# Performance work log

Measured on AMD Instinct MI355X. Metric: run time of the kernel, lower is better.

## Reference

```python
import jax, jax.numpy as jnp
import numpy as np

EPS = 1e-7   # GENConv message eps
LN_EPS = 1e-5


def _ln(x, g, b):
    mu = jnp.mean(x, axis=-1, keepdims=True)
    var = jnp.mean((x - mu) ** 2, axis=-1, keepdims=True)
    return (x - mu) * jax.lax.rsqrt(var + LN_EPS) * g + b


def _genconv(h, e, src, dst, W1, b1, g1, bt1, W2, b2, t):
    # GENConv with softmax aggregation and 2-layer MLP (Linear->LN->ReLU->Linear)
    N = h.shape[0]
    m = jax.nn.relu(h[src] + e) + EPS                  # [E,H] messages
    logit = m * t
    mx = jax.ops.segment_max(logit, dst, num_segments=N)   # per-dst, per-channel max
    ex = jnp.exp(logit - mx[dst])
    den = jax.ops.segment_sum(ex, dst, num_segments=N)
    alpha = ex / jnp.maximum(den[dst], 1e-16)          # per-dst softmax weights
    agg = jax.ops.segment_sum(m * alpha, dst, num_segments=N)
    z = agg + h                                        # out + x_r
    z = jnp.dot(z, W1.T) + b1                          # [N,2H]
    z = jax.nn.relu(_ln(z, g1, bt1))
    return jnp.dot(z, W2.T) + b2                       # [N,H]


def setup_inputs() -> dict:
    key = jax.random.key(0)
    ks = jax.random.split(key, 10)
    B, S, H, L, deg = 16, 4096, 64, 4, 16
    N = B * S
    E = N * deg  # 65536 edges per sample, repeated structure
    x = jax.random.normal(ks[0], (N,), jnp.float32)
    edge_index = jax.random.randint(ks[1], (2, E), 0, N)
    edge_attr = jax.random.normal(ks[2], (E,), jnp.float32)
    batch = jnp.repeat(jnp.arange(B, dtype=jnp.int32), S)

    def nrm(k, shape, fan_in):
        return jax.random.normal(k, shape, jnp.float32) / np.float32(np.sqrt(fan_in))

    return dict(
        x=x, edge_index=edge_index, edge_attr=edge_attr, batch=batch, input_size=S,
        node_W=nrm(ks[3], (H, 1), 1), node_b=jnp.zeros((H,), jnp.float32),
        edge_W=nrm(ks[4], (H, 1), 1), edge_b=jnp.zeros((H,), jnp.float32),
        conv_W1=nrm(ks[5], (L, 2 * H, H), H), conv_b1=jnp.zeros((L, 2 * H), jnp.float32),
        conv_lng=jnp.ones((L, 2 * H), jnp.float32), conv_lnb=jnp.zeros((L, 2 * H), jnp.float32),
        conv_W2=nrm(ks[6], (L, H, 2 * H), 2 * H), conv_b2=jnp.zeros((L, H), jnp.float32),
        conv_t=jnp.ones((L,), jnp.float32),
        ln_g=jnp.ones((L, H), jnp.float32), ln_b=jnp.zeros((L, H), jnp.float32),
        lin_W=nrm(ks[7], (1, S * H), S * H), lin_b=jnp.zeros((1,), jnp.float32),
    )


def reference(x, edge_index, edge_attr, batch, input_size,
              node_W, node_b, edge_W, edge_b,
              conv_W1, conv_b1, conv_lng, conv_lnb, conv_W2, conv_b2, conv_t,
              ln_g, ln_b, lin_W, lin_b):
    N = x.shape[0]
    B = N // input_size
    src, dst = edge_index[0], edge_index[1]
    # node encoder: Linear(1,H) applied to every scalar node feature (batched GEMV)
    h = x[:, None] * node_W[:, 0][None, :] + node_b    # [N,H]
    # edge encoder: only row 0 of reshaped edge_attr is encoded, then repeated B times
    ea0 = edge_attr.reshape(B, -1)[0]                  # [E/B]
    eenc = ea0[:, None] * edge_W[:, 0][None, :] + edge_b
    e = jnp.tile(eenc, (B, 1))                         # [E,H]
    L = conv_W1.shape[0]
    # layer 0: conv only
    h = _genconv(h, e, src, dst, conv_W1[0], conv_b1[0], conv_lng[0], conv_lnb[0],
                 conv_W2[0], conv_b2[0], conv_t[0])
    # layers 1..L-1: res+ blocks (norm -> relu -> [dropout disabled, eval] -> conv -> residual)
    for l in range(1, L):
        hh = jax.nn.relu(_ln(h, ln_g[l], ln_b[l]))
        hh = _genconv(hh, e, src, dst, conv_W1[l], conv_b1[l], conv_lng[l], conv_lnb[l],
                      conv_W2[l], conv_b2[l], conv_t[l])
        h = h + hh
    h = jax.nn.relu(_ln(h, ln_g[0], ln_b[0]))
    # per-sample flatten + Linear readout (batch ids are contiguous blocks)
    y = h.reshape(B, -1) @ lin_W.T + lin_b             # [B,1]
    return y.reshape(-1)                               # [B]
```

## Files before the change

kernel.cpp:

```cpp
#include <hip/hip_runtime.h>

namespace {

typedef __attribute__((ext_vector_type(8))) short bf16x8;
typedef __attribute__((ext_vector_type(4))) float f32x4;

constexpr int NN = 65536;
constexpr int NE = 1 << 20;
constexpr int H2 = 128;
constexpr int NL = 4;
constexpr float GEPS = 1e-7f;
constexpr float LNEPS = 1e-5f;
constexpr float LOG2E = 1.44269504088896340736f;

__device__ inline unsigned f2bf(float f) {
  unsigned u = __builtin_bit_cast(unsigned, f);
  return (u + 0x7fffu + ((u >> 16) & 1u)) >> 16;
}
__device__ inline float bf2f(unsigned b) {
  unsigned u = b << 16;
  return __builtin_bit_cast(float, u);
}

__global__ __launch_bounds__(256) void kA0(const int* __restrict__ dst,
                                           int* __restrict__ bcnt) {
  __shared__ int h[256];
  int t = threadIdx.x;
  h[t] = 0;
  __syncthreads();
  int bs = blockIdx.x * 4096;
#pragma unroll 4
  for (int i = 0; i < 16; ++i) {
    int d = dst[bs + i * 256 + t];
    atomicAdd(&h[d >> 8], 1);
  }
  __syncthreads();
  atomicAdd(&bcnt[t], h[t]);
}

__global__ __launch_bounds__(256) void kScanB(const int* __restrict__ bcnt,
                                              int* __restrict__ bbase,
                                              int* __restrict__ cursorA) {
  __shared__ int s[256];
  int t = threadIdx.x;
  int v = bcnt[t];
  s[t] = v;
  __syncthreads();
  for (int dd = 1; dd < 256; dd <<= 1) {
    int val = (t >= dd) ? s[t - dd] : 0;
    __syncthreads();
    s[t] += val;
    __syncthreads();
  }
  int ex = s[t] - v;
  bbase[t] = ex;
  cursorA[t] = ex;
  if (t == 255) bbase[256] = NE;
}

__global__ __launch_bounds__(256) void kA1(const int* __restrict__ src,
                                           const int* __restrict__ dst,
                                           const float* __restrict__ ea0,
                                           int* __restrict__ cursorA,
                                           uint2* __restrict__ binned) {
  __shared__ int h[256], lcur[256], base[256];
  int t = threadIdx.x;
  h[t] = 0;
  lcur[t] = 0;
  __syncthreads();
  int bs = blockIdx.x * 4096;
#pragma unroll 4
  for (int i = 0; i < 16; ++i) {
    int d = dst[bs + i * 256 + t];
    atomicAdd(&h[d >> 8], 1);
  }
  __syncthreads();
  base[t] = atomicAdd(&cursorA[t], h[t]);
  __syncthreads();
  for (int i = 0; i < 16; ++i) {
    int e = bs + i * 256 + t;
    int d = dst[e];
    int s = src[e];
    float a = ea0[e & 65535];
    int b = d >> 8;
    int k = atomicAdd(&lcur[b], 1);
    uint2 r;
    r.x = (unsigned)s | ((unsigned)(d & 255) << 16);
    r.y = __builtin_bit_cast(unsigned, a);
    binned[base[b] + k] = r;
  }
}

__global__ __launch_bounds__(256) void kB(const uint2* __restrict__ binned,
                                          const int* __restrict__ bbase,
                                          uint2* __restrict__ recs,
                                          int* __restrict__ offsets) {
  __shared__ int h[256], sc[256], ex[256], lcur[256];
  int t = threadIdx.x;
  int b = blockIdx.x;
  int s0 = bbase[b], s1 = bbase[b + 1], n = s1 - s0;
  h[t] = 0;
  lcur[t] = 0;
  __syncthreads();
  for (int i = t; i < n; i += 256) atomicAdd(&h[(binned[s0 + i].x >> 16) & 255], 1);
  __syncthreads();
  sc[t] = h[t];
  __syncthreads();
  for (int dd = 1; dd < 256; dd <<= 1) {
    int val = (t >= dd) ? sc[t - dd] : 0;
    __syncthreads();
    sc[t] += val;
    __syncthreads();
  }
  ex[t] = sc[t] - h[t];
  offsets[b * 256 + t] = s0 + ex[t];
  if (b == 0 && t == 0) offsets[NN] = NE;
  __syncthreads();
  for (int i = t; i < n; i += 256) {
    uint2 r = binned[s0 + i];
    int d8 = (r.x >> 16) & 255;
    int k = atomicAdd(&lcur[d8], 1);
    uint2 o;
    o.x = r.x & 0xffffu;
    o.y = r.y;
    recs[s0 + ex[d8] + k] = o;
  }
}

template <int L0>
__global__ __launch_bounds__(256) void k_agg(const unsigned short* __restrict__ hinb,
                                             const float* __restrict__ hinf,
                                             const float* __restrict__ x,
                                             const float* __restrict__ nW,
                                             const float* __restrict__ nb,
                                             const float* __restrict__ eW,
                                             const float* __restrict__ eb,
                                             const int* __restrict__ offsets,
                                             const uint2* __restrict__ recs,
                                             const float* __restrict__ conv_t, int layer,
                                             float* __restrict__ zbuf) {
  int lane = threadIdx.x & 63;
  int d = blockIdx.x * 4 + (threadIdx.x >> 6);
  float t2 = conv_t[layer] * LOG2E;
  float eWl = eW[lane], ebl = eb[lane];
  float nWl = 0.f, nbl = 0.f;
  if (L0) { nWl = nW[lane]; nbl = nb[lane]; }
  int off = __builtin_amdgcn_readfirstlane(offsets[d]);
  int end = __builtin_amdgcn_readfirstlane(offsets[d + 1]);
  float hself = L0 ? fmaf(x[d], nWl, nbl) : hinf[d * 64 + lane];
  const uint2* rp = recs + off;
  int n = end - off;

  auto edgeval = [&](int k) -> float {
    uint2 r = rp[k];
    int s = __builtin_amdgcn_readfirstlane((int)r.x);
    float a = __builtin_bit_cast(float, __builtin_amdgcn_readfirstlane((int)r.y));
    float ec = fmaf(a, eWl, ebl);
    float hs = L0 ? fmaf(x[s], nWl, nbl) : bf2f(hinb[s * 64 + lane]);
    return fmaxf(hs + ec, 0.f) + GEPS;
  };

  float den0 = 0.f, num0 = 0.f, den1 = 0.f, num1 = 0.f;
  int k = 0;
  for (; k + 4 <= n; k += 4) {
    float m0 = edgeval(k), m1 = edgeval(k + 1), m2 = edgeval(k + 2), m3 = edgeval(k + 3);
    float e0 = exp2f(m0 * t2), e1 = exp2f(m1 * t2);
    float e2 = exp2f(m2 * t2), e3 = exp2f(m3 * t2);
    den0 += e0 + e1;
    den1 += e2 + e3;
    num0 += fmaf(m0, e0, m1 * e1);
    num1 += fmaf(m2, e2, m3 * e3);
  }
  for (; k < n; ++k) {
    float m = edgeval(k);
    float e = exp2f(m * t2);
    den0 += e;
    num0 = fmaf(m, e, num0);
  }
  float den = den0 + den1, num = num0 + num1;
  float agg = num / fmaxf(den, 1e-16f);
  zbuf[d * 64 + lane] = agg + hself;
}

__global__ __launch_bounds__(256) void k_wprep(const float* __restrict__ W1,
                                               const float* __restrict__ W2,
                                               unsigned short* __restrict__ w1hi,
                                               unsigned short* __restrict__ w1lo,
                                               unsigned short* __restrict__ w2hi,
                                               unsigned short* __restrict__ w2lo) {
  int t = blockIdx.x * 256 + threadIdx.x;
  int which = t >> 15;
  int o = t & 32767;
  int l = o >> 13, idx = o & 8191;
  int fid = idx >> 9, lane = (idx >> 3) & 63, j = idx & 7;
  int lr = lane & 15, lg = lane >> 4;
  if (which == 0) {
    int nt = fid >> 1, ks = fid & 1;
    int m = nt * 16 + lr, k = ks * 32 + lg * 8 + j;
    float v = W1[l * 8192 + m * 64 + k];
    unsigned hi = f2bf(v);
    w1hi[o] = (unsigned short)hi;
    w1lo[o] = (unsigned short)f2bf(v - bf2f(hi));
  } else {
    int mt = fid >> 2, ks = fid & 3;
    int m = mt * 16 + lr, k = ks * 32 + lg * 8 + j;
    float v = W2[l * 8192 + m * 128 + k];
    unsigned hi = f2bf(v);
    w2hi[o] = (unsigned short)hi;
    w2lo[o] = (unsigned short)f2bf(v - bf2f(hi));
  }
}

__global__ __launch_bounds__(256) void k_mlpmm(const float* __restrict__ zbuf,
                                               float* __restrict__ h,
                                               float* __restrict__ hinf,
                                               unsigned short* __restrict__ hinb,
                                               const unsigned short* __restrict__ w1hi,
                                               const unsigned short* __restrict__ w1lo,
                                               const unsigned short* __restrict__ w2hi,
                                               const unsigned short* __restrict__ w2lo,
                                               const float* __restrict__ b1,
                                               const float* __restrict__ g1,
                                               const float* __restrict__ bt1,
                                               const float* __restrict__ b2,
                                               const float* __restrict__ gnx,
                                               const float* __restrict__ bnx,
                                               const float* __restrict__ linW,
                                               float* __restrict__ partials,
                                               int mode) {
  __shared__ unsigned Yb[4][16 * 132];
  int tid = threadIdx.x, wv = tid >> 6, l = tid & 63;
  int lr = l & 15, lg = l >> 4;
  unsigned* Y = Yb[wv];
  int n0 = (blockIdx.x * 4 + wv) * 16;

  bf16x8 zh[2], zl[2];
#pragma unroll
  for (int ks = 0; ks < 2; ++ks) {
    const float* zp = zbuf + (n0 + lr) * 64 + ks * 32 + lg * 8;
    float4 a = *(const float4*)zp, b = *(const float4*)(zp + 4);
    float zv[8] = {a.x, a.y, a.z, a.w, b.x, b.y, b.z, b.w};
    bf16x8 hh, ll;
#pragma unroll
    for (int j = 0; j < 8; ++j) {
      unsigned hi = f2bf(zv[j]);
      hh[j] = (short)hi;
      ll[j] = (short)f2bf(zv[j] - bf2f(hi));
    }
    zh[ks] = hh;
    zl[ks] = ll;
  }

  f32x4 C1[8];
#pragma unroll
  for (int nt = 0; nt < 8; ++nt) {
    bf16x8 a0h = *(const bf16x8*)(w1hi + ((nt * 2 + 0) * 64 + l) * 8);
    bf16x8 a0l = *(const bf16x8*)(w1lo + ((nt * 2 + 0) * 64 + l) * 8);
    bf16x8 a1h = *(const bf16x8*)(w1hi + ((nt * 2 + 1) * 64 + l) * 8);
    bf16x8 a1l = *(const bf16x8*)(w1lo + ((nt * 2 + 1) * 64 + l) * 8);
    f32x4 c = {0.f, 0.f, 0.f, 0.f};
    c = __builtin_amdgcn_mfma_f32_16x16x32_bf16(a0h, zh[0], c, 0, 0, 0);
    c = __builtin_amdgcn_mfma_f32_16x16x32_bf16(a0l, zh[0], c, 0, 0, 0);
    c = __builtin_amdgcn_mfma_f32_16x16x32_bf16(a0h, zl[0], c, 0, 0, 0);
    c = __builtin_amdgcn_mfma_f32_16x16x32_bf16(a1h, zh[1], c, 0, 0, 0);
    c = __builtin_amdgcn_mfma_f32_16x16x32_bf16(a1l, zh[1], c, 0, 0, 0);
    c = __builtin_amdgcn_mfma_f32_16x16x32_bf16(a1h, zl[1], c, 0, 0, 0);
    C1[nt] = c;
  }

  float s = 0.f, q = 0.f;
#pragma unroll
  for (int nt = 0; nt < 8; ++nt) {
    float4 bv = *(const float4*)(b1 + nt * 16 + lg * 4);
#pragma unroll
    for (int r = 0; r < 4; ++r) {
      float v = C1[nt][r] + ((const float*)&bv)[r];
      C1[nt][r] = v;
      s += v;
      q += v * v;
    }
  }
  s += __shfl_xor(s, 16); q += __shfl_xor(q, 16);
  s += __shfl_xor(s, 32); q += __shfl_xor(q, 32);
  float mu = s * (1.f / 128.f);
  float rs = rsqrtf(q * (1.f / 128.f) - mu * mu + LNEPS);
#pragma unroll
  for (int nt = 0; nt < 8; ++nt) {
    float4 gv = *(const float4*)(g1 + nt * 16 + lg * 4);
    float4 btv = *(const float4*)(bt1 + nt * 16 + lg * 4);
    unsigned pk[4];
#pragma unroll
    for (int r = 0; r < 4; ++r) {
      float y = fmaxf((C1[nt][r] - mu) * rs * ((const float*)&gv)[r] + ((const float*)&btv)[r], 0.f);
      unsigned hi = f2bf(y);
      unsigned lo = f2bf(y - bf2f(hi));
      pk[r] = hi | (lo << 16);
    }
    int idx = lr * 132 + ((nt * 16 + lg * 4) ^ ((lr & 7) << 2));
    *(uint4*)(Y + idx) = make_uint4(pk[0], pk[1], pk[2], pk[3]);
  }

  bf16x8 yh[4], yl[4];
#pragma unroll
  for (int ks = 0; ks < 4; ++ks) {
    bf16x8 hh, ll;
#pragma unroll
    for (int half = 0; half < 2; ++half) {
      int cb = ks * 32 + lg * 8 + half * 4;
      uint4 v = *(const uint4*)(Y + lr * 132 + (cb ^ ((lr & 7) << 2)));
      unsigned dw[4] = {v.x, v.y, v.z, v.w};
#pragma unroll
      for (int j = 0; j < 4; ++j) {
        hh[half * 4 + j] = (short)(dw[j] & 0xffffu);
        ll[half * 4 + j] = (short)(dw[j] >> 16);
      }
    }
    yh[ks] = hh;
    yl[ks] = ll;
  }

  f32x4 C2[4];
#pragma unroll
  for (int mt = 0; mt < 4; ++mt) {
    f32x4 c = {0.f, 0.f, 0.f, 0.f};
#pragma unroll
    for (int ks = 0; ks < 4; ++ks) {
      bf16x8 ah = *(const bf16x8*)(w2hi + ((mt * 4 + ks) * 64 + l) * 8);
      bf16x8 al = *(const bf16x8*)(w2lo + ((mt * 4 + ks) * 64 + l) * 8);
      c = __builtin_amdgcn_mfma_f32_16x16x32_bf16(ah, yh[ks], c, 0, 0, 0);
      c = __builtin_amdgcn_mfma_f32_16x16x32_bf16(al, yh[ks], c, 0, 0, 0);
      c = __builtin_amdgcn_mfma_f32_16x16x32_bf16(ah, yl[ks], c, 0, 0, 0);
    }
    C2[mt] = c;
  }

  int gnode = n0 + lr;
  float s2 = 0.f, q2 = 0.f;
#pragma unroll
  for (int mt = 0; mt < 4; ++mt) {
    float4 b2v = *(const float4*)(b2 + mt * 16 + lg * 4);
    float4 hr = {0.f, 0.f, 0.f, 0.f};
    if (mode != 0) hr = *(const float4*)(h + gnode * 64 + mt * 16 + lg * 4);
    float4 hv;
#pragma unroll
    for (int r = 0; r < 4; ++r) {
      float o = C2[mt][r] + ((const float*)&b2v)[r];
      float v = (mode == 0) ? o : ((const float*)&hr)[r] + o;
      ((float*)&hv)[r] = v;
      s2 += v;
      q2 += v * v;
      C2[mt][r] = v;
    }
    if (mode != 2) *(float4*)(h + gnode * 64 + mt * 16 + lg * 4) = hv;
  }
  s2 += __shfl_xor(s2, 16); q2 += __shfl_xor(q2, 16);
  s2 += __shfl_xor(s2, 32); q2 += __shfl_xor(q2, 32);
  float mu2 = s2 * (1.f / 64.f);
  float rs2 = rsqrtf(q2 * (1.f / 64.f) - mu2 * mu2 + LNEPS);
  if (mode != 2) {
#pragma unroll
    for (int mt = 0; mt < 4; ++mt) {
      float4 gv = *(const float4*)(gnx + mt * 16 + lg * 4);
      float4 bv = *(const float4*)(bnx + mt * 16 + lg * 4);
      float4 fo;
#pragma unroll
      for (int r = 0; r < 4; ++r)
        ((float*)&fo)[r] = fmaxf((C2[mt][r] - mu2) * rs2 * ((const float*)&gv)[r] + ((const float*)&bv)[r], 0.f);
      *(float4*)(hinf + gnode * 64 + mt * 16 + lg * 4) = fo;
      uint2 pb;
      pb.x = f2bf(fo.x) | (f2bf(fo.y) << 16);
      pb.y = f2bf(fo.z) | (f2bf(fo.w) << 16);
      *(uint2*)(hinb + gnode * 64 + mt * 16 + lg * 4) = pb;
    }
  } else {
    float p = 0.f;
#pragma unroll
    for (int mt = 0; mt < 4; ++mt) {
      float4 gv = *(const float4*)(gnx + mt * 16 + lg * 4);
      float4 bv = *(const float4*)(bnx + mt * 16 + lg * 4);
      float4 lw = *(const float4*)(linW + (gnode & 4095) * 64 + mt * 16 + lg * 4);
#pragma unroll
      for (int r = 0; r < 4; ++r) {
        float f = fmaxf((C2[mt][r] - mu2) * rs2 * ((const float*)&gv)[r] + ((const float*)&bv)[r], 0.f);
        p += f * ((const float*)&lw)[r];
      }
    }
    p += __shfl_xor(p, 16);
    p += __shfl_xor(p, 32);
    if (lg == 0) partials[gnode] = p;
  }
}

__global__ __launch_bounds__(256) void k_readout2(const float* __restrict__ partials,
                                                  const float* __restrict__ linb,
                                                  float* __restrict__ out) {
  __shared__ float s[256];
  int b = blockIdx.x, t = threadIdx.x;
  float acc = 0.0f;
  for (int i = t; i < 4096; i += 256) acc += partials[b * 4096 + i];
  s[t] = acc;
  __syncthreads();
  for (int d = 128; d > 0; d >>= 1) {
    if (t < d) s[t] += s[t + d];
    __syncthreads();
  }
  if (t == 0) out[b] = s[0] + linb[0];
}

}

extern "C" void kernel_launch(void* const* d_in, const int* in_sizes, int n_in,
                              void* d_out, int out_size, void* d_ws, size_t ws_size,
                              hipStream_t stream) {
  const float* x = (const float*)d_in[0];
  const int* ei = (const int*)d_in[1];
  const float* ea = (const float*)d_in[2];
  const float* nW = (const float*)d_in[5];
  const float* nb = (const float*)d_in[6];
  const float* eW = (const float*)d_in[7];
  const float* eb = (const float*)d_in[8];
  const float* W1 = (const float*)d_in[9];
  const float* b1 = (const float*)d_in[10];
  const float* g1 = (const float*)d_in[11];
  const float* bt1 = (const float*)d_in[12];
  const float* W2 = (const float*)d_in[13];
  const float* b2 = (const float*)d_in[14];
  const float* ct = (const float*)d_in[15];
  const float* lng = (const float*)d_in[16];
  const float* lnb = (const float*)d_in[17];
  const float* linW = (const float*)d_in[18];
  const float* linb = (const float*)d_in[19];
  float* out = (float*)d_out;

  const int* src = ei;
  const int* dst = ei + NE;

  char* p = (char*)d_ws;
  auto alloc = [&](size_t bytes) {
    char* r = p;
    p += (bytes + 255) & ~size_t(255);
    return r;
  };
  float* h = (float*)alloc(size_t(NN) * 64 * 4);
  float* hinf = (float*)alloc(size_t(NN) * 64 * 4);
  unsigned short* hinb = (unsigned short*)alloc(size_t(NN) * 64 * 2);
  float* zbuf = (float*)alloc(size_t(NN) * 64 * 4);
  uint2* binned = (uint2*)alloc(size_t(NE) * 8);
  uint2* recs = (uint2*)alloc(size_t(NE) * 8);
  int* offsets = (int*)alloc(size_t(NN + 1) * 4);
  int* bcnt = (int*)alloc(256 * 4);
  int* bbase = (int*)alloc(257 * 4);
  int* cursorA = (int*)alloc(256 * 4);
  float* partials = (float*)alloc(size_t(NN) * 4);
  unsigned short* w1hi = (unsigned short*)alloc(4 * 8192 * 2);
  unsigned short* w1lo = (unsigned short*)alloc(4 * 8192 * 2);
  unsigned short* w2hi = (unsigned short*)alloc(4 * 8192 * 2);
  unsigned short* w2lo = (unsigned short*)alloc(4 * 8192 * 2);

  k_wprep<<<256, 256, 0, stream>>>(W1, W2, w1hi, w1lo, w2hi, w2lo);

  hipMemsetAsync(bcnt, 0, 256 * 4, stream);
  kA0<<<256, 256, 0, stream>>>(dst, bcnt);
  kScanB<<<1, 256, 0, stream>>>(bcnt, bbase, cursorA);
  kA1<<<256, 256, 0, stream>>>(src, dst, ea, cursorA, binned);
  kB<<<256, 256, 0, stream>>>(binned, bbase, recs, offsets);

  for (int l = 0; l < NL; ++l) {
    if (l == 0)
      k_agg<1><<<NN / 4, 256, 0, stream>>>(hinb, hinf, x, nW, nb, eW, eb,
                                           offsets, recs, ct, l, zbuf);
    else
      k_agg<0><<<NN / 4, 256, 0, stream>>>(hinb, hinf, x, nW, nb, eW, eb,
                                           offsets, recs, ct, l, zbuf);
    int mode = (l == 0) ? 0 : (l == NL - 1 ? 2 : 1);
    const float* gnext = (l == NL - 1) ? lng : lng + (l + 1) * 64;
    const float* bnext = (l == NL - 1) ? lnb : lnb + (l + 1) * 64;
    k_mlpmm<<<NN / 64, 256, 0, stream>>>(zbuf, h, hinf, hinb,
                                         w1hi + l * 8192, w1lo + l * 8192,
                                         w2hi + l * 8192, w2lo + l * 8192,
                                         b1 + l * H2, g1 + l * H2, bt1 + l * H2,
                                         b2 + l * 64, gnext, bnext,
                                         linW, partials, mode);
  }

  k_readout2<<<16, 256, 0, stream>>>(partials, linb, out);
}
```

Before: 313.1 us.

## Switch aggregation to edge-parallel segmented reduction with atomics, fold finalize into MLP

Replaces the per-destination-node aggregation (one wavefront per node walking its CSR range) with an edge-parallel kernel where each wavefront takes 64 sorted edges, does a segmented reduction over runs of equal destination, and flushes den/num partials via global float atomics. The division num/den and the self-term add move into the MLP kernel, which also re-zeroes the accumulators for the next layer. The aim is to remove load imbalance from variable node degrees and the offsets array. In exchange it adds two full-size accumulator buffers, atomic traffic, and nondeterministic float summation order.

Result: slower. 339.6 us (+8.5%).

```diff
diff --git a/kernel.cpp b/kernel.cpp
--- a/kernel.cpp
+++ b/kernel.cpp
@@ -93,8 +93,7 @@
 
 __global__ __launch_bounds__(256) void kB(const uint2* __restrict__ binned,
                                           const int* __restrict__ bbase,
-                                          uint2* __restrict__ recs,
-                                          int* __restrict__ offsets) {
+                                          uint2* __restrict__ recs) {
   __shared__ int h[256], sc[256], ex[256], lcur[256];
   int t = threadIdx.x;
   int b = blockIdx.x;
@@ -113,73 +112,76 @@
     __syncthreads();
   }
   ex[t] = sc[t] - h[t];
-  offsets[b * 256 + t] = s0 + ex[t];
-  if (b == 0 && t == 0) offsets[NN] = NE;
   __syncthreads();
   for (int i = t; i < n; i += 256) {
     uint2 r = binned[s0 + i];
     int d8 = (r.x >> 16) & 255;
     int k = atomicAdd(&lcur[d8], 1);
     uint2 o;
-    o.x = r.x & 0xffffu;
+    o.x = (r.x & 0xffffu) | ((unsigned)(b * 256 + d8) << 16);
     o.y = r.y;
     recs[s0 + ex[d8] + k] = o;
   }
 }
 
 template <int L0>
-__global__ __launch_bounds__(256) void k_agg(const unsigned short* __restrict__ hinb,
-                                             const float* __restrict__ hinf,
-                                             const float* __restrict__ x,
-                                             const float* __restrict__ nW,
-                                             const float* __restrict__ nb,
-                                             const float* __restrict__ eW,
-                                             const float* __restrict__ eb,
-                                             const int* __restrict__ offsets,
-                                             const uint2* __restrict__ recs,
-                                             const float* __restrict__ conv_t, int layer,
-                                             float* __restrict__ zbuf) {
-  int lane = threadIdx.x & 63;
-  int d = blockIdx.x * 4 + (threadIdx.x >> 6);
+__global__ __launch_bounds__(256) void k_aggE(const unsigned short* __restrict__ hinb,
+                                              const float* __restrict__ x,
+                                              const float* __restrict__ nW,
+                                              const float* __restrict__ nb,
+                                              const float* __restrict__ eW,
+                                              const float* __restrict__ eb,
+                                              const uint2* __restrict__ recs,
+                                              const float* __restrict__ conv_t, int layer,
+                                              float* __restrict__ deng,
+                                              float* __restrict__ numg) {
+  __shared__ uint2 rs[4][64];
+  int wv = threadIdx.x >> 6, lane = threadIdx.x & 63;
+  int e0 = (blockIdx.x * 4 + wv) * 64;
+  rs[wv][lane] = recs[e0 + lane];
+  __syncthreads();
+
   float t2 = conv_t[layer] * LOG2E;
   float eWl = eW[lane], ebl = eb[lane];
   float nWl = 0.f, nbl = 0.f;
   if (L0) { nWl = nW[lane]; nbl = nb[lane]; }
-  int off = __builtin_amdgcn_readfirstlane(offsets[d]);
-  int end = __builtin_amdgcn_readfirstlane(offsets[d + 1]);
-  float hself = L0 ? fmaf(x[d], nWl, nbl) : hinf[d * 64 + lane];
-  const uint2* rp = recs + off;
-  int n = end - off;
-
-  auto edgeval = [&](int k) -> float {
-    uint2 r = rp[k];
-    int s = __builtin_amdgcn_readfirstlane((int)r.x);
-    float a = __builtin_bit_cast(float, __builtin_amdgcn_readfirstlane((int)r.y));
-    float ec = fmaf(a, eWl, ebl);
-    float hs = L0 ? fmaf(x[s], nWl, nbl) : bf2f(hinb[s * 64 + lane]);
-    return fmaxf(hs + ec, 0.f) + GEPS;
-  };
-
-  float den0 = 0.f, num0 = 0.f, den1 = 0.f, num1 = 0.f;
-  int k = 0;
-  for (; k + 4 <= n; k += 4) {
-    float m0 = edgeval(k), m1 = edgeval(k + 1), m2 = edgeval(k + 2), m3 = edgeval(k + 3);
-    float e0 = exp2f(m0 * t2), e1 = exp2f(m1 * t2);
-    float e2 = exp2f(m2 * t2), e3 = exp2f(m3 * t2);
-    den0 += e0 + e1;
-    den1 += e2 + e3;
-    num0 += fmaf(m0, e0, m1 * e1);
-    num1 += fmaf(m2, e2, m3 * e3);
-  }
-  for (; k < n; ++k) {
-    float m = edgeval(k);
-    float e = exp2f(m * t2);
-    den0 += e;
-    num0 = fmaf(m, e, num0);
-  }
-  float den = den0 + den1, num = num0 + num1;
-  float agg = num / fmaxf(den, 1e-16f);
-  zbuf[d * 64 + lane] = agg + hself;
+
+  int curd = -1;
+  float den = 0.f, num = 0.f;
+#pragma unroll 2
+  for (int k0 = 0; k0 < 64; k0 += 8) {
+    float m[8], e[8];
+    int dd[8];
+#pragma unroll
+    for (int j = 0; j < 8; ++j) {
+      uint2 r = rs[wv][k0 + j];
+      unsigned rx = (unsigned)__builtin_amdgcn_readfirstlane((int)r.x);
+      float a = __builtin_bit_cast(float, __builtin_amdgcn_readfirstlane((int)r.y));
+      int sk = (int)(rx & 0xffffu);
+      dd[j] = (int)(rx >> 16);
+      float hs = L0 ? fmaf(x[sk], nWl, nbl) : bf2f(hinb[sk * 64 + lane]);
+      float mm = fmaxf(fmaf(a, eWl, ebl) + hs, 0.f) + GEPS;
+      m[j] = mm;
+      e[j] = exp2f(mm * t2);
+    }
+#pragma unroll
+    for (int j = 0; j < 8; ++j) {
+      if (dd[j] != curd) {
+        if (curd >= 0) {
+          atomicAdd(&deng[curd * 64 + lane], den);
+          atomicAdd(&numg[curd * 64 + lane], num);
+        }
+        curd = dd[j];
+        den = e[j];
+        num = m[j] * e[j];
+      } else {
+        den += e[j];
+        num = fmaf(m[j], e[j], num);
+      }
+    }
+  }
+  atomicAdd(&deng[curd * 64 + lane], den);
+  atomicAdd(&numg[curd * 64 + lane], num);
 }
 
 __global__ __launch_bounds__(256) void k_wprep(const float* __restrict__ W1,
@@ -211,7 +213,11 @@
   }
 }
 
-__global__ __launch_bounds__(256) void k_mlpmm(const float* __restrict__ zbuf,
+__global__ __launch_bounds__(256) void k_mlpmm(float* __restrict__ deng,
+                                               float* __restrict__ numg,
+                                               const float* __restrict__ x,
+                                               const float* __restrict__ nodeW,
+                                               const float* __restrict__ nodeB,
                                                float* __restrict__ h,
                                                float* __restrict__ hinf,
                                                unsigned short* __restrict__ hinb,
@@ -233,19 +239,42 @@
   int lr = l & 15, lg = l >> 4;
   unsigned* Y = Yb[wv];
   int n0 = (blockIdx.x * 4 + wv) * 16;
-
+  int node = n0 + lr;
+
+  float xv = 0.f;
+  if (mode == 0) xv = x[node];
   bf16x8 zh[2], zl[2];
+  const float4 zero4 = {0.f, 0.f, 0.f, 0.f};
 #pragma unroll
   for (int ks = 0; ks < 2; ++ks) {
-    const float* zp = zbuf + (n0 + lr) * 64 + ks * 32 + lg * 8;
-    float4 a = *(const float4*)zp, b = *(const float4*)(zp + 4);
-    float zv[8] = {a.x, a.y, a.z, a.w, b.x, b.y, b.z, b.w};
+    int c0 = ks * 32 + lg * 8;
+    float* dp = deng + node * 64 + c0;
+    float* np = numg + node * 64 + c0;
+    float4 da = *(const float4*)dp, db = *(const float4*)(dp + 4);
+    float4 na = *(const float4*)np, nb4 = *(const float4*)(np + 4);
+    float dv[8] = {da.x, da.y, da.z, da.w, db.x, db.y, db.z, db.w};
+    float nv[8] = {na.x, na.y, na.z, na.w, nb4.x, nb4.y, nb4.z, nb4.w};
+    float hv[8];
+    if (mode == 0) {
+#pragma unroll
+      for (int j = 0; j < 8; ++j) hv[j] = fmaf(xv, nodeW[c0 + j], nodeB[c0 + j]);
+    } else {
+      float4 ha = *(const float4*)(hinf + node * 64 + c0);
+      float4 hb = *(const float4*)(hinf + node * 64 + c0 + 4);
+      hv[0] = ha.x; hv[1] = ha.y; hv[2] = ha.z; hv[3] = ha.w;
+      hv[4] = hb.x; hv[5] = hb.y; hv[6] = hb.z; hv[7] = hb.w;
+    }
+    *(float4*)dp = zero4;
+    *(float4*)(dp + 4) = zero4;
+    *(float4*)np = zero4;
+    *(float4*)(np + 4) = zero4;
     bf16x8 hh, ll;
 #pragma unroll
     for (int j = 0; j < 8; ++j) {
-      unsigned hi = f2bf(zv[j]);
+      float zv = nv[j] / fmaxf(dv[j], 1e-16f) + hv[j];
+      unsigned hi = f2bf(zv);
       hh[j] = (short)hi;
-      ll[j] = (short)f2bf(zv[j] - bf2f(hi));
+      ll[j] = (short)f2bf(zv - bf2f(hi));
     }
     zh[ks] = hh;
     zl[ks] = ll;
@@ -334,7 +363,7 @@
     C2[mt] = c;
   }
 
-  int gnode = n0 + lr;
+  int gnode = node;
   float s2 = 0.f, q2 = 0.f;
 #pragma unroll
   for (int mt = 0; mt < 4; ++mt) {
@@ -444,10 +473,10 @@
   float* h = (float*)alloc(size_t(NN) * 64 * 4);
   float* hinf = (float*)alloc(size_t(NN) * 64 * 4);
   unsigned short* hinb = (unsigned short*)alloc(size_t(NN) * 64 * 2);
-  float* zbuf = (float*)alloc(size_t(NN) * 64 * 4);
+  float* deng = (float*)alloc(size_t(NN) * 64 * 4);
+  float* numg = (float*)alloc(size_t(NN) * 64 * 4);
   uint2* binned = (uint2*)alloc(size_t(NE) * 8);
   uint2* recs = (uint2*)alloc(size_t(NE) * 8);
-  int* offsets = (int*)alloc(size_t(NN + 1) * 4);
   int* bcnt = (int*)alloc(256 * 4);
   int* bbase = (int*)alloc(257 * 4);
   int* cursorA = (int*)alloc(256 * 4);
@@ -459,23 +488,26 @@
 
   k_wprep<<<256, 256, 0, stream>>>(W1, W2, w1hi, w1lo, w2hi, w2lo);
 
+  hipMemsetAsync(deng, 0, size_t(NN) * 64 * 4, stream);
+  hipMemsetAsync(numg, 0, size_t(NN) * 64 * 4, stream);
+
   hipMemsetAsync(bcnt, 0, 256 * 4, stream);
   kA0<<<256, 256, 0, stream>>>(dst, bcnt);
   kScanB<<<1, 256, 0, stream>>>(bcnt, bbase, cursorA);
   kA1<<<256, 256, 0, stream>>>(src, dst, ea, cursorA, binned);
-  kB<<<256, 256, 0, stream>>>(binned, bbase, recs, offsets);
+  kB<<<256, 256, 0, stream>>>(binned, bbase, recs);
 
   for (int l = 0; l < NL; ++l) {
     if (l == 0)
-      k_agg<1><<<NN / 4, 256, 0, stream>>>(hinb, hinf, x, nW, nb, eW, eb,
-                                           offsets, recs, ct, l, zbuf);
+      k_aggE<1><<<NE / 256, 256, 0, stream>>>(hinb, x, nW, nb, eW, eb,
+                                              recs, ct, l, deng, numg);
     else
-      k_agg<0><<<NN / 4, 256, 0, stream>>>(hinb, hinf, x, nW, nb, eW, eb,
-                                           offsets, recs, ct, l, zbuf);
+      k_aggE<0><<<NE / 256, 256, 0, stream>>>(hinb, x, nW, nb, eW, eb,
+                                              recs, ct, l, deng, numg);
     int mode = (l == 0) ? 0 : (l == NL - 1 ? 2 : 1);
     const float* gnext = (l == NL - 1) ? lng : lng + (l + 1) * 64;
     const float* bnext = (l == NL - 1) ? lnb : lnb + (l + 1) * 64;
-    k_mlpmm<<<NN / 64, 256, 0, stream>>>(zbuf, h, hinf, hinb,
+    k_mlpmm<<<NN / 64, 256, 0, stream>>>(deng, numg, x, nW, nb, h, hinf, hinb,
                                          w1hi + l * 8192, w1lo + l * 8192,
                                          w2hi + l * 8192, w2lo + l * 8192,
                                          b1 + l * H2, g1 + l * H2, bt1 + l * H2,
```
